# Performance work log

Hardware: AMD Instinct MI355X
Metric: run time of the kernel (lower is better)

Reference implementation:

```python
import jax, jax.numpy as jnp
import numpy as np
import itertools


def _identity_grid(n, d, h, w, dtype):
    # Replicates AffineGridGenerator with identity theta:
    # linspace(-1,1,K) per axis (align_corners=True convention),
    # grid[..., 0]=x(W), grid[...,1]=y(H), grid[...,2]=z(D).
    zs = jnp.linspace(-1.0, 1.0, d, dtype=dtype) if d > 1 else jnp.array([-1.0], dtype=dtype)
    ys = jnp.linspace(-1.0, 1.0, h, dtype=dtype) if h > 1 else jnp.array([-1.0], dtype=dtype)
    xs = jnp.linspace(-1.0, 1.0, w, dtype=dtype) if w > 1 else jnp.array([-1.0], dtype=dtype)
    gz, gy, gx = jnp.meshgrid(zs, ys, xs, indexing='ij')  # [D,H,W]
    grid = jnp.stack([gx, gy, gz], axis=-1)               # [D,H,W,3]
    return jnp.broadcast_to(grid, (n, d, h, w, 3))


def _trilinear_sample(x, grid):
    N, C, Din, Hin, Win = x.shape
    dt = x.dtype
    fx = (grid[..., 0] + 1.0) * 0.5 * (Win - 1)
    fy = (grid[..., 1] + 1.0) * 0.5 * (Hin - 1)
    fz = (grid[..., 2] + 1.0) * 0.5 * (Din - 1)
    x0 = jnp.floor(fx); y0 = jnp.floor(fy); z0 = jnp.floor(fz)
    wx1 = (fx - x0).astype(dt); wy1 = (fy - y0).astype(dt); wz1 = (fz - z0).astype(dt)
    wx = (1.0 - wx1, wx1); wy = (1.0 - wy1, wy1); wz = (1.0 - wz1, wz1)
    ix = (x0.astype(jnp.int32), x0.astype(jnp.int32) + 1)
    iy = (y0.astype(jnp.int32), y0.astype(jnp.int32) + 1)
    iz = (z0.astype(jnp.int32), z0.astype(jnp.int32) + 1)

    def gather(xb, izb, iyb, ixb):
        return xb[:, izb, iyb, ixb]  # [C,D,H,W]
    gather_b = jax.vmap(gather)

    out = jnp.zeros((N, C) + grid.shape[1:4], dtype=dt)
    for a, b, c in itertools.product((0, 1), repeat=3):  # (z,y,x) corner
        zi, yi, xi = iz[a], iy[b], ix[c]
        valid = ((zi >= 0) & (zi < Din) & (yi >= 0) & (yi < Hin)
                 & (xi >= 0) & (xi < Win))
        zi = jnp.clip(zi, 0, Din - 1)
        yi = jnp.clip(yi, 0, Hin - 1)
        xi = jnp.clip(xi, 0, Win - 1)
        wgt = (wz[a] * wy[b] * wx[c]) * valid.astype(dt)  # [N,D,H,W]
        vals = gather_b(x, zi, yi, xi)                     # [N,C,D,H,W]
        out = out + vals * wgt[:, None]
    return out


def reference(x, d_out, h_out, w_out, variance):
    if variance:
        x = jnp.exp(x / 2.0)
    grid = _identity_grid(x.shape[0], d_out, h_out, w_out, x.dtype)
    out = _trilinear_sample(x, grid)
    if variance:
        out = jnp.log(out) * 2.0
    return out


def setup_inputs() -> dict:
    key = jax.random.key(0)
    x = jax.random.normal(key, (8, 32, 32, 64, 64), dtype=jnp.float32)
    return {"x": x, "d_out": 48, "h_out": 96, "w_out": 96, "variance": 1}
```

## Files before the change

### kernel.cpp

```cpp
#include <hip/hip_runtime.h>

constexpr int N = 8, C = 32, Din = 32, Hin = 64, Win = 64;
constexpr int Do = 48, Ho = 96, Wo = 96;

constexpr int BLOCK        = 256;
constexpr int NBLOCKS      = N * C * Do;
constexpr int WAVES        = BLOCK / 64;
constexpr int ROWS_PER_WAVE = Ho / WAVES;

__global__ __launch_bounds__(BLOCK)
void resample3d_var_kernel(const float* __restrict__ in, float* __restrict__ out) {
    __shared__ float G[Hin][Win];

    const int bid = blockIdx.x;
    const int zo  = bid % Do;
    const int nc  = bid / Do;

    float fz = (float)(zo * (Din - 1)) / (float)(Do - 1);
    int   z0 = (int)fz;
    float wz1 = fz - (float)z0;
    int   z1 = min(z0 + 1, Din - 1);
    float wz0 = 1.0f - wz1;

    const float* __restrict__ p0 = in + ((size_t)nc * Din + z0) * (Hin * Win);
    const float* __restrict__ p1 = in + ((size_t)nc * Din + z1) * (Hin * Win);

    const int tid = threadIdx.x;
    const int sy  = tid >> 4;
    const int sx  = (tid & 15) << 2;
#pragma unroll
    for (int k = 0; k < 4; ++k) {
        int y = sy + k * 16;
        const float4 a = *reinterpret_cast<const float4*>(p0 + y * Win + sx);
        const float4 b = *reinterpret_cast<const float4*>(p1 + y * Win + sx);
        float4 g;
        g.x = wz0 * __expf(a.x * 0.5f) + wz1 * __expf(b.x * 0.5f);
        g.y = wz0 * __expf(a.y * 0.5f) + wz1 * __expf(b.y * 0.5f);
        g.z = wz0 * __expf(a.z * 0.5f) + wz1 * __expf(b.z * 0.5f);
        g.w = wz0 * __expf(a.w * 0.5f) + wz1 * __expf(b.w * 0.5f);
        *reinterpret_cast<float4*>(&G[y][sx]) = g;
    }
    __syncthreads();

    const int wave = tid >> 6;
    const int lane = tid & 63;

    int xoA = lane;
    int xoB = 64 + (lane & 31);
    float fxA = (float)(xoA * (Win - 1)) / (float)(Wo - 1);
    float fxB = (float)(xoB * (Win - 1)) / (float)(Wo - 1);
    int   x0A = (int)fxA;  float wxA = fxA - (float)x0A;
    int   x0B = (int)fxB;  float wxB = fxB - (float)x0B;
    int   aA0 = x0A << 2;
    int   aA1 = min(x0A + 1, Win - 1) << 2;
    int   aB0 = x0B << 2;
    int   aB1 = min(x0B + 1, Win - 1) << 2;

    const int yo0 = wave * ROWS_PER_WAVE;
    float* op = out + (((size_t)nc * Do + zo) * Ho + yo0) * Wo;

    constexpr float TWO_LN2 = 1.3862943611198906f;

    for (int r = 0; r < ROWS_PER_WAVE; ++r) {
        int   yo = yo0 + r;
        float fy = (float)(yo * (Hin - 1)) / (float)(Ho - 1);
        int   y0 = (int)fy;
        float wy1 = fy - (float)y0;
        int   y1 = min(y0 + 1, Hin - 1);

        float g0 = G[y0][lane];
        float g1 = G[y1][lane];
        float F  = g0 + wy1 * (g1 - g0);

        int Fi = __builtin_bit_cast(int, F);
        float FA0 = __builtin_bit_cast(float, __builtin_amdgcn_ds_bpermute(aA0, Fi));
        float FA1 = __builtin_bit_cast(float, __builtin_amdgcn_ds_bpermute(aA1, Fi));
        float vA  = FA0 + wxA * (FA1 - FA0);
        op[lane] = TWO_LN2 * __log2f(vA);

        float FB0 = __builtin_bit_cast(float, __builtin_amdgcn_ds_bpermute(aB0, Fi));
        float FB1 = __builtin_bit_cast(float, __builtin_amdgcn_ds_bpermute(aB1, Fi));
        float vB  = FB0 + wxB * (FB1 - FB0);
        if (lane < 32) op[64 + lane] = TWO_LN2 * __log2f(vB);

        op += Wo;
    }
}

extern "C" void kernel_launch(void* const* d_in, const int* in_sizes, int n_in,
                              void* d_out, int out_size, void* d_ws, size_t ws_size,
                              hipStream_t stream) {
    const float* x = (const float*)d_in[0];
    float* out = (float*)d_out;
    resample3d_var_kernel<<<NBLOCKS, BLOCK, 0, stream>>>(x, out);
}
```

Baseline: 130.3 us.

## Stage y-interpolated rows in LDS and emit float4 output stores

Replaces the per-row wave-permute x-interpolation with a two-phase scheme. First the y-interpolated rows for half the output plane are written into a padded shared buffer. Then each thread reads its x-neighbours from that buffer and writes four contiguous outputs as one float4 store. The goal is wider, fully coalesced stores in place of the partially masked scalar row stores and bpermute traffic. In exchange it adds extra LDS round trips and barriers, and the ratio divides are replaced by reciprocal multiplies, which may shift float rounding of the indices.

```diff
diff --git a/kernel.cpp b/kernel.cpp
--- a/kernel.cpp
+++ b/kernel.cpp
@@ -3,87 +3,94 @@
 constexpr int N = 8, C = 32, Din = 32, Hin = 64, Win = 64;
 constexpr int Do = 48, Ho = 96, Wo = 96;
 
-constexpr int BLOCK        = 256;
-constexpr int NBLOCKS      = N * C * Do;
-constexpr int WAVES        = BLOCK / 64;
-constexpr int ROWS_PER_WAVE = Ho / WAVES;
+constexpr int BLOCK   = 256;
+constexpr int NBLOCKS = N * C * Do;
+constexpr int HROWS   = Ho / 2;
+constexpr int F2PAD   = 68;
+constexpr int QUADS   = HROWS * (Wo / 4);
 
 __global__ __launch_bounds__(BLOCK)
 void resample3d_var_kernel(const float* __restrict__ in, float* __restrict__ out) {
     __shared__ float G[Hin][Win];
+    __shared__ float F2[HROWS][F2PAD];
 
+    const int tid = threadIdx.x;
     const int bid = blockIdx.x;
     const int zo  = bid % Do;
     const int nc  = bid / Do;
 
-    float fz = (float)(zo * (Din - 1)) / (float)(Do - 1);
-    int   z0 = (int)fz;
+    float fz  = (float)(zo * (Din - 1)) * (1.0f / (float)(Do - 1));
+    int   z0  = (int)fz;
     float wz1 = fz - (float)z0;
-    int   z1 = min(z0 + 1, Din - 1);
+    int   z1  = min(z0 + 1, Din - 1);
     float wz0 = 1.0f - wz1;
 
     const float* __restrict__ p0 = in + ((size_t)nc * Din + z0) * (Hin * Win);
     const float* __restrict__ p1 = in + ((size_t)nc * Din + z1) * (Hin * Win);
 
-    const int tid = threadIdx.x;
-    const int sy  = tid >> 4;
-    const int sx  = (tid & 15) << 2;
+    {
+        const int sy = tid >> 4;
+        const int sx = (tid & 15) << 2;
 #pragma unroll
-    for (int k = 0; k < 4; ++k) {
-        int y = sy + k * 16;
-        const float4 a = *reinterpret_cast<const float4*>(p0 + y * Win + sx);
-        const float4 b = *reinterpret_cast<const float4*>(p1 + y * Win + sx);
-        float4 g;
-        g.x = wz0 * __expf(a.x * 0.5f) + wz1 * __expf(b.x * 0.5f);
-        g.y = wz0 * __expf(a.y * 0.5f) + wz1 * __expf(b.y * 0.5f);
-        g.z = wz0 * __expf(a.z * 0.5f) + wz1 * __expf(b.z * 0.5f);
-        g.w = wz0 * __expf(a.w * 0.5f) + wz1 * __expf(b.w * 0.5f);
-        *reinterpret_cast<float4*>(&G[y][sx]) = g;
+        for (int k = 0; k < 4; ++k) {
+            int y = sy + k * 16;
+            const float4 a = *reinterpret_cast<const float4*>(p0 + y * Win + sx);
+            const float4 b = *reinterpret_cast<const float4*>(p1 + y * Win + sx);
+            float4 g;
+            g.x = wz0 * __expf(a.x * 0.5f) + wz1 * __expf(b.x * 0.5f);
+            g.y = wz0 * __expf(a.y * 0.5f) + wz1 * __expf(b.y * 0.5f);
+            g.z = wz0 * __expf(a.z * 0.5f) + wz1 * __expf(b.z * 0.5f);
+            g.w = wz0 * __expf(a.w * 0.5f) + wz1 * __expf(b.w * 0.5f);
+            *reinterpret_cast<float4*>(&G[y][sx]) = g;
+        }
     }
     __syncthreads();
 
-    const int wave = tid >> 6;
-    const int lane = tid & 63;
-
-    int xoA = lane;
-    int xoB = 64 + (lane & 31);
-    float fxA = (float)(xoA * (Win - 1)) / (float)(Wo - 1);
-    float fxB = (float)(xoB * (Win - 1)) / (float)(Wo - 1);
-    int   x0A = (int)fxA;  float wxA = fxA - (float)x0A;
-    int   x0B = (int)fxB;  float wxB = fxB - (float)x0B;
-    int   aA0 = x0A << 2;
-    int   aA1 = min(x0A + 1, Win - 1) << 2;
-    int   aB0 = x0B << 2;
-    int   aB1 = min(x0B + 1, Win - 1) << 2;
-
-    const int yo0 = wave * ROWS_PER_WAVE;
-    float* op = out + (((size_t)nc * Do + zo) * Ho + yo0) * Wo;
-
+    const size_t obase = ((size_t)nc * Do + zo) * (size_t)(Ho * Wo);
     constexpr float TWO_LN2 = 1.3862943611198906f;
 
-    for (int r = 0; r < ROWS_PER_WAVE; ++r) {
-        int   yo = yo0 + r;
-        float fy = (float)(yo * (Hin - 1)) / (float)(Ho - 1);
-        int   y0 = (int)fy;
-        float wy1 = fy - (float)y0;
-        int   y1 = min(y0 + 1, Hin - 1);
+    for (int h = 0; h < 2; ++h) {
+        {
+            const int x   = tid & 63;
+            const int yr0 = tid >> 6;
+#pragma unroll
+            for (int j = 0; j < 12; ++j) {
+                int yrow = j * 4 + yr0;
+                int yo   = h * HROWS + yrow;
+                float fy  = (float)(yo * (Hin - 1)) * (1.0f / (float)(Ho - 1));
+                int   y0  = (int)fy;
+                float wy1 = fy - (float)y0;
+                int   y1  = min(y0 + 1, Hin - 1);
+                float g0 = G[y0][x], g1 = G[y1][x];
+                F2[yrow][x] = g0 + wy1 * (g1 - g0);
+            }
+        }
+        __syncthreads();
 
-        float g0 = G[y0][lane];
-        float g1 = G[y1][lane];
-        float F  = g0 + wy1 * (g1 - g0);
-
-        int Fi = __builtin_bit_cast(int, F);
-        float FA0 = __builtin_bit_cast(float, __builtin_amdgcn_ds_bpermute(aA0, Fi));
-        float FA1 = __builtin_bit_cast(float, __builtin_amdgcn_ds_bpermute(aA1, Fi));
-        float vA  = FA0 + wxA * (FA1 - FA0);
-        op[lane] = TWO_LN2 * __log2f(vA);
-
-        float FB0 = __builtin_bit_cast(float, __builtin_amdgcn_ds_bpermute(aB0, Fi));
-        float FB1 = __builtin_bit_cast(float, __builtin_amdgcn_ds_bpermute(aB1, Fi));
-        float vB  = FB0 + wxB * (FB1 - FB0);
-        if (lane < 32) op[64 + lane] = TWO_LN2 * __log2f(vB);
-
-        op += Wo;
+        float* __restrict__ ob = out + obase + (size_t)h * (HROWS * Wo);
+#pragma unroll
+        for (int k = 0; k < 5; ++k) {
+            int c = k * BLOCK + tid;
+            if (c < QUADS) {
+                int row = (c * 2731) >> 16;
+                int q   = c - row * 24;
+                float4 o;
+                float* op = &o.x;
+#pragma unroll
+                for (int i = 0; i < 4; ++i) {
+                    int   xo  = q * 4 + i;
+                    float fx  = (float)(xo * (Win - 1)) * (1.0f / (float)(Wo - 1));
+                    int   x0  = (int)fx;
+                    float wx1 = fx - (float)x0;
+                    int   x1  = min(x0 + 1, Win - 1);
+                    float F0 = F2[row][x0], F1 = F2[row][x1];
+                    float v  = F0 + wx1 * (F1 - F0);
+                    op[i] = TWO_LN2 * __log2f(v);
+                }
+                *reinterpret_cast<float4*>(ob + (size_t)c * 4) = o;
+            }
+        }
+        if (h == 0) __syncthreads();
     }
 }
 
```

Result: faster. 124.9 us (-4.1%).
